# Performance work log

Hardware: AMD Instinct MI355X
Metric: run time of the kernel (lower is better)

## Reference

```python
import jax, jax.numpy as jnp
import numpy as np

NEG_SLOPE = 0.01  # torch F.leaky_relu default
N_USER = 100000
N_ITEM = 100000
N_EDGE = 640000
D = 128
N_LAYERS = 3  # 1 input + num_hidden_layers(1) + 1 output layer


def setup_inputs() -> dict:
    key = jax.random.key(0)
    ks = jax.random.split(key, 10)
    scale = 1.0 / np.sqrt(D)
    return {
        "h_user": jax.random.normal(ks[0], (N_USER, D), dtype=jnp.float32),
        "h_item": jax.random.normal(ks[1], (N_ITEM, D), dtype=jnp.float32),
        # W[layer, etype] : etype 0 = user-follows->user, 1 = user-clicks->item, 2 = item-clicked_by->user
        "W": jax.random.normal(ks[2], (N_LAYERS, 3, D, D), dtype=jnp.float32) * scale,
        "b": jnp.zeros((N_LAYERS, 3, D), dtype=jnp.float32),
        "follows_src": jax.random.randint(ks[3], (N_EDGE,), 0, N_USER, dtype=jnp.int32),
        "follows_dst": jax.random.randint(ks[4], (N_EDGE,), 0, N_USER, dtype=jnp.int32),
        "clicks_src": jax.random.randint(ks[5], (N_EDGE,), 0, N_USER, dtype=jnp.int32),
        "clicks_dst": jax.random.randint(ks[6], (N_EDGE,), 0, N_ITEM, dtype=jnp.int32),
        "cb_src": jax.random.randint(ks[7], (N_EDGE,), 0, N_ITEM, dtype=jnp.int32),
        "cb_dst": jax.random.randint(ks[8], (N_EDGE,), 0, N_USER, dtype=jnp.int32),
    }


def _etype_conv(h_src, W, b, src, dst, n_dst):
    """Per-etype Linear on src nodes, copy_u gather, mean-aggregate at dst."""
    Wh = h_src @ W + b                     # [N_src, D] dense transform (once per node)
    msg = Wh[src]                          # [E, D] gather
    s = jax.ops.segment_sum(msg, dst, num_segments=n_dst)
    cnt = jax.ops.segment_sum(jnp.ones((src.shape[0],), dtype=Wh.dtype), dst, num_segments=n_dst)
    return s / jnp.maximum(cnt, 1.0)[:, None]  # mean; isolated nodes -> 0


def _rgcn_forward(h_user, h_item, W, b, follows_src, follows_dst,
                  clicks_src, clicks_dst, cb_src, cb_dst):
    hu, hi = h_user, h_item
    for l in range(N_LAYERS):
        # per-etype mean aggregation, then cross-etype 'sum' (DGL multi_update_all)
        agg_u = (_etype_conv(hu, W[l, 0], b[l, 0], follows_src, follows_dst, N_USER)
                 + _etype_conv(hi, W[l, 2], b[l, 2], cb_src, cb_dst, N_USER))
        agg_i = _etype_conv(hu, W[l, 1], b[l, 1], clicks_src, clicks_dst, N_ITEM)
        hu = jax.nn.leaky_relu(agg_u, NEG_SLOPE)
        hi = jax.nn.leaky_relu(agg_i, NEG_SLOPE)
    return jnp.stack([hu, hi])  # [2, 100000, 128]


def reference(h_user, h_item, W, b, follows_src, follows_dst,
              clicks_src, clicks_dst, cb_src, cb_dst):
    return _rgcn_forward(h_user, h_item, W, b, follows_src, follows_dst,
                         clicks_src, clicks_dst, cb_src, cb_dst)
```

## Files before the change

kernel.cpp:

```cpp
#include <hip/hip_runtime.h>

typedef unsigned char u8;
typedef unsigned short u16;
typedef _Float16 f16;
typedef __attribute__((ext_vector_type(4))) _Float16 f16x4;
typedef __attribute__((ext_vector_type(8))) _Float16 f16x8;
typedef __attribute__((ext_vector_type(4))) float f32x4;

#define D 128
#define PG 4

__global__ __launch_bounds__(256) void k_pre(
    const float* __restrict__ h_user, const float* __restrict__ h_item,
    const float* __restrict__ W,
    const int* __restrict__ fd, const int* __restrict__ cd,
    const int* __restrict__ cbd,
    u16* __restrict__ h_all, u16* __restrict__ Wtg,
    int* __restrict__ cnt, u8* __restrict__ pos,
    int NU, int NI, int nf, int nc, int ncb,
    int nbCnt, int nbCvtU, int nbCvtI) {
  int b = blockIdx.x;
  int T = gridDim.x;
  long before = (long)b * nbCnt / T;
  long after = (long)(b + 1) * nbCnt / T;
  if (after > before) {
    int e = (int)before * 256 + threadIdx.x;
    int d;
    if (e < nf)
      d = fd[e];
    else if (e < nf + nc)
      d = NU + cd[e - nf];
    else if (e < nf + nc + ncb)
      d = NU + NI + cbd[e - nf - nc];
    else
      return;
    int p = atomicAdd(&cnt[d], 1);
    pos[e] = (u8)p;
  } else {
    int v = b - (int)before;
    if (v < nbCvtU + nbCvtI) {
      bool isU = v < nbCvtU;
      int i = (isU ? v : v - nbCvtU) * 256 + threadIdx.x;
      int n8 = (isU ? NU : NI) * 16;
      if (i >= n8) return;
      const float4* ip = (const float4*)(isU ? h_user : h_item);
      u16* op = h_all + (isU ? 0 : (size_t)NU * D);
      float4 a = ip[i * 2], c = ip[i * 2 + 1];
      f16x8 vv = {(f16)a.x, (f16)a.y, (f16)a.z, (f16)a.w,
                  (f16)c.x, (f16)c.y, (f16)c.z, (f16)c.w};
      *(f16x8*)(op + (size_t)i * 8) = vv;
    } else {
      int idx = (v - nbCvtU - nbCvtI) * 256 + threadIdx.x;
      if (idx >= 9 * 16384) return;
      int mat = idx >> 14;
      int k = (idx >> 7) & 127;
      int n = idx & 127;
      ((f16*)Wtg)[(size_t)mat * 16384 + n * 128 + k] = (f16)W[idx];
    }
  }
}

__device__ __forceinline__ int pad4(int x) { return (x + (PG - 1)) & ~(PG - 1); }

__global__ __launch_bounds__(256) void k_scanA(const int* __restrict__ cnt,
                                               int* __restrict__ part, int n) {
  int t = threadIdx.x;
  int idx = blockIdx.x * 1024 + t * 4;
  int s = 0;
  if (idx + 3 < n) {
    int4 c = *(const int4*)(cnt + idx);
    s = pad4(c.x) + pad4(c.y) + pad4(c.z) + pad4(c.w);
  } else {
#pragma unroll
    for (int j = 0; j < 4; ++j)
      if (idx + j < n) s += pad4(cnt[idx + j]);
  }
  for (int off = 1; off < 64; off <<= 1) s += __shfl_down(s, off, 64);
  __shared__ int ws[4];
  if ((t & 63) == 0) ws[t >> 6] = s;
  __syncthreads();
  if (t == 0) part[blockIdx.x] = ws[0] + ws[1] + ws[2] + ws[3];
}

__global__ __launch_bounds__(1024) void k_scanB(int* __restrict__ part, int n_part) {
  __shared__ int sh[1024];
  int t = threadIdx.x;
  int v = (t < n_part) ? part[t] : 0;
  sh[t] = v;
  __syncthreads();
  for (int off = 1; off < 1024; off <<= 1) {
    int u = (t >= off) ? sh[t - off] : 0;
    __syncthreads();
    sh[t] += u;
    __syncthreads();
  }
  if (t < n_part) part[t] = sh[t] - v;
}

__global__ __launch_bounds__(256) void k_scanC(const int* __restrict__ cnt,
                                               const int* __restrict__ part,
                                               int* __restrict__ rs, int n) {
  int t = threadIdx.x;
  int idx = blockIdx.x * 1024 + t * 4;
  int v0 = 0, v1 = 0, v2 = 0, v3 = 0;
  if (idx + 3 < n) {
    int4 c = *(const int4*)(cnt + idx);
    v0 = pad4(c.x);
    v1 = pad4(c.y);
    v2 = pad4(c.z);
    v3 = pad4(c.w);
  } else {
    if (idx < n) v0 = pad4(cnt[idx]);
    if (idx + 1 < n) v1 = pad4(cnt[idx + 1]);
    if (idx + 2 < n) v2 = pad4(cnt[idx + 2]);
    if (idx + 3 < n) v3 = pad4(cnt[idx + 3]);
  }
  int s = v0 + v1 + v2 + v3;
  int inc = s;
  int lane = t & 63, w = t >> 6;
  for (int off = 1; off < 64; off <<= 1) {
    int u = __shfl_up(inc, off, 64);
    if (lane >= off) inc += u;
  }
  __shared__ int ws[4];
  if (lane == 63) ws[w] = inc;
  __syncthreads();
  int woff = 0;
  for (int i = 0; i < w; ++i) woff += ws[i];
  int ex = part[blockIdx.x] + woff + inc - s;
  int4 r;
  r.x = ex;
  r.y = ex + v0;
  r.z = r.y + v1;
  r.w = r.z + v2;
  if (idx + 3 < n)
    *(int4*)(rs + idx) = r;
  else {
    if (idx < n) rs[idx] = r.x;
    if (idx + 1 < n) rs[idx + 1] = r.y;
    if (idx + 2 < n) rs[idx + 2] = r.z;
    if (idx + 3 < n) rs[idx + 3] = r.w;
  }
  if (idx <= n - 1 && n - 1 < idx + 4) {
    int j = n - 1 - idx;
    int incl = (j == 0) ? r.x + v0 : (j == 1) ? r.y + v1 : (j == 2) ? r.z + v2 : r.w + v3;
    rs[n] = incl;
  }
}

__global__ __launch_bounds__(256) void k_fill2(
    const int* __restrict__ fs, const int* __restrict__ fd,
    const int* __restrict__ cs, const int* __restrict__ cd,
    const int* __restrict__ cbs, const int* __restrict__ cbd,
    const int* __restrict__ rs, const int* __restrict__ cnt,
    const u8* __restrict__ pos, int* __restrict__ csr,
    int NU, int NI, int nf, int nc, int ncb, int nbFill, int N3, int ZR) {
  if ((int)blockIdx.x < nbFill) {
    int e = blockIdx.x * 256 + threadIdx.x;
    int d, s;
    if (e < nf) {
      d = fd[e];
      s = fs[e];
    } else if (e < nf + nc) {
      d = NU + cd[e - nf];
      s = cs[e - nf];
    } else if (e < nf + nc + ncb) {
      d = NU + NI + cbd[e - nf - nc];
      s = cbs[e - nf - nc] + NU;
    } else
      return;
    csr[rs[d] + (int)pos[e]] = s;
  } else {
    int d = (blockIdx.x - nbFill) * 256 + threadIdx.x;
    if (d >= N3) return;
    int deg = cnt[d];
    int degp = pad4(deg);
    int base = rs[d] + deg;
#pragma unroll
    for (int j = 0; j < PG - 1; ++j)
      if (j < degp - deg) csr[base + j] = ZR;
  }
}

__global__ __launch_bounds__(256) void k_agg3(
    const u16* __restrict__ h_all, const int* __restrict__ csr,
    const int* __restrict__ rs, const int* __restrict__ cnt,
    u16* __restrict__ M_all, int N3) {
  int wave = (blockIdx.x * 256 + threadIdx.x) >> 6;
  int lane = threadIdx.x & 63;
  int l16 = lane & 15;
  int w = wave * 4 + (lane >> 4);
  bool valid = w < N3;
  int wc = valid ? w : 0;
  int e = rs[wc];
  int en = valid ? rs[wc + 1] : e;
  int deg = valid ? cnt[wc] : 0;
  f16x8 acc0 = {0, 0, 0, 0, 0, 0, 0, 0};
  f16x8 acc1 = {0, 0, 0, 0, 0, 0, 0, 0};
  const char* hb = (const char*)h_all;
  const int4* csr4 = (const int4*)csr;
  unsigned loff = (unsigned)l16 * 16u;

  int en8 = e + ((en - e) & ~7);
  while (e < en8) {
    int4 c0 = csr4[e >> 2];
    int4 c1 = csr4[(e >> 2) + 1];
    f16x8 v0 = *(const f16x8*)(hb + ((unsigned)c0.x * 256u + loff));
    f16x8 v1 = *(const f16x8*)(hb + ((unsigned)c0.y * 256u + loff));
    f16x8 v2 = *(const f16x8*)(hb + ((unsigned)c0.z * 256u + loff));
    f16x8 v3 = *(const f16x8*)(hb + ((unsigned)c0.w * 256u + loff));
    f16x8 v4 = *(const f16x8*)(hb + ((unsigned)c1.x * 256u + loff));
    f16x8 v5 = *(const f16x8*)(hb + ((unsigned)c1.y * 256u + loff));
    f16x8 v6 = *(const f16x8*)(hb + ((unsigned)c1.z * 256u + loff));
    f16x8 v7 = *(const f16x8*)(hb + ((unsigned)c1.w * 256u + loff));
    acc0 += v0;
    acc1 += v1;
    acc0 += v2;
    acc1 += v3;
    acc0 += v4;
    acc1 += v5;
    acc0 += v6;
    acc1 += v7;
    e += 8;
  }
  if (e < en) {
    int4 c0 = csr4[e >> 2];
    f16x8 v0 = *(const f16x8*)(hb + ((unsigned)c0.x * 256u + loff));
    f16x8 v1 = *(const f16x8*)(hb + ((unsigned)c0.y * 256u + loff));
    f16x8 v2 = *(const f16x8*)(hb + ((unsigned)c0.z * 256u + loff));
    f16x8 v3 = *(const f16x8*)(hb + ((unsigned)c0.w * 256u + loff));
    acc0 += v0;
    acc1 += v1;
    acc0 += v2;
    acc1 += v3;
  }

  if (valid) {
    float invf = deg > 0 ? 1.0f / (float)deg : 0.f;
    f16 hinv = (f16)invf;
    f16x8 t = acc0 + acc1;
    f16x8 r = t * hinv;
    *(f16x8*)((char*)M_all + ((unsigned)wc * 256u + loff)) = r;
  }
}

template <int NE, int OUTF32>
__device__ __forceinline__ void gemm_body(
    const u16* __restrict__ mA, const u16* __restrict__ mBp,
    const u16* __restrict__ wtA, const u16* __restrict__ wtB,
    const float* __restrict__ bA, const float* __restrict__ bB,
    const int* __restrict__ cntA, const int* __restrict__ cntB,
    u16* __restrict__ o16, float* __restrict__ o32, int M, int blk) {
  int tid = threadIdx.x, lane = tid & 63, w = tid >> 6;
  int lr = lane & 15;
  int lk = (lane >> 4) * 8;
  long row0 = (long)blk * 128 + w * 32;

  f32x4 acc[2][8];
#pragma unroll
  for (int rt = 0; rt < 2; rt++)
#pragma unroll
    for (int n = 0; n < 8; n++) acc[rt][n] = (f32x4){0.f, 0.f, 0.f, 0.f};

#pragma unroll
  for (int e = 0; e < NE; ++e) {
    const f16* mm = (const f16*)((e == 0) ? mA : mBp);
    const f16* Wg = (const f16*)((e == 0) ? wtA : wtB);
#pragma unroll
    for (int ks = 0; ks < 4; ++ks) {
      int k0 = ks * 32 + lk;
      f16x8 bf[8];
#pragma unroll
      for (int n = 0; n < 8; n++) bf[n] = *(const f16x8*)(Wg + (n * 16 + lr) * D + k0);
#pragma unroll
      for (int rt = 0; rt < 2; rt++) {
        long r = row0 + rt * 16 + lr;
        if (r >= M) r = M - 1;
        f16x8 af = *(const f16x8*)(mm + r * D + k0);
#pragma unroll
        for (int n = 0; n < 8; n++)
          acc[rt][n] = __builtin_amdgcn_mfma_f32_16x16x32_f16(bf[n], af, acc[rt][n], 0, 0, 0);
      }
    }
  }

  int g4 = (lane >> 4) * 4;
  float4 bAr[8], bBr[8];
#pragma unroll
  for (int n = 0; n < 8; n++) {
    bAr[n] = *(const float4*)&bA[n * 16 + g4];
    if (NE == 2) bBr[n] = *(const float4*)&bB[n * 16 + g4];
  }

#pragma unroll
  for (int rt = 0; rt < 2; rt++) {
    long r = row0 + rt * 16 + lr;
    if (r < M) {
      bool mAok = cntA[r] > 0;
      bool mBok = (NE == 2) && (cntB[r] > 0);
#pragma unroll
      for (int n = 0; n < 8; n++) {
        float4 vv;
        vv.x = acc[rt][n][0];
        vv.y = acc[rt][n][1];
        vv.z = acc[rt][n][2];
        vv.w = acc[rt][n][3];
        if (mAok) {
          vv.x += bAr[n].x;
          vv.y += bAr[n].y;
          vv.z += bAr[n].z;
          vv.w += bAr[n].w;
        }
        if (mBok) {
          vv.x += bBr[n].x;
          vv.y += bBr[n].y;
          vv.z += bBr[n].z;
          vv.w += bBr[n].w;
        }
        vv.x = vv.x > 0.f ? vv.x : 0.01f * vv.x;
        vv.y = vv.y > 0.f ? vv.y : 0.01f * vv.y;
        vv.z = vv.z > 0.f ? vv.z : 0.01f * vv.z;
        vv.w = vv.w > 0.f ? vv.w : 0.01f * vv.w;
        int col = n * 16 + g4;
        if (OUTF32) {
          *(float4*)&o32[r * D + col] = vv;
        } else {
          f16x4 h = {(f16)vv.x, (f16)vv.y, (f16)vv.z, (f16)vv.w};
          *(f16x4*)((f16*)o16 + r * D + col) = h;
        }
      }
    }
  }
}

template <int OUTF32>
__global__ __launch_bounds__(256) void k_gemm2(
    const u16* __restrict__ M_all, const u16* __restrict__ Wl,
    const float* __restrict__ bl, const int* __restrict__ cnt,
    u16* __restrict__ h_all, float* __restrict__ out,
    int NU, int NI, int nbI) {
  if ((int)blockIdx.x < nbI) {
    gemm_body<1, OUTF32>(M_all + (size_t)NU * D, nullptr,
                         Wl + 16384, nullptr,
                         bl + D, nullptr,
                         cnt + NU, nullptr,
                         h_all + (size_t)NU * D, out + (size_t)NU * D, NI,
                         blockIdx.x);
  } else {
    gemm_body<2, OUTF32>(M_all, M_all + (size_t)(NU + NI) * D,
                         Wl, Wl + 2 * 16384,
                         bl, bl + 2 * D,
                         cnt, cnt + NU + NI,
                         h_all, out, NU, blockIdx.x - nbI);
  }
}

extern "C" void kernel_launch(void* const* d_in, const int* in_sizes, int n_in,
                              void* d_out, int out_size, void* d_ws, size_t ws_size,
                              hipStream_t stream) {
  const float* h_user = (const float*)d_in[0];
  const float* h_item = (const float*)d_in[1];
  const float* W = (const float*)d_in[2];
  const float* bb = (const float*)d_in[3];
  const int* f_src = (const int*)d_in[4];
  const int* f_dst = (const int*)d_in[5];
  const int* c_src = (const int*)d_in[6];
  const int* c_dst = (const int*)d_in[7];
  const int* cb_src = (const int*)d_in[8];
  const int* cb_dst = (const int*)d_in[9];

  const int NU = in_sizes[0] / D;
  const int NI = in_sizes[1] / D;
  const int nEf = in_sizes[4], nEc = in_sizes[6], nEcb = in_sizes[8];
  const int N3 = NU + NI + NU;
  const int nE = nEf + nEc + nEcb;
  const int ZR = NU + NI;

  char* p = (char*)d_ws;
  auto alloc = [&](size_t bytes) {
    char* r = p;
    p += (bytes + 255) & ~(size_t)255;
    return r;
  };
  int* cnt = (int*)alloc((size_t)N3 * 4);
  int* rs_all = (int*)alloc((size_t)(N3 + 1) * 4);
  int* part = (int*)alloc(1024 * 4);
  u16* Wtg = (u16*)alloc((size_t)9 * 16384 * 2);
  int* csr_all = (int*)alloc(((size_t)nE + (size_t)(PG - 1) * N3) * 4);
  u16* h_all = (u16*)alloc((size_t)(NU + NI + 1) * D * 2);
  u16* M_all = (u16*)alloc((size_t)N3 * D * 2);
  u8* pos = (u8*)M_all;
  (void)ws_size;

  hipMemsetAsync(cnt, 0, (size_t)N3 * 4, stream);
  hipMemsetAsync(h_all + (size_t)ZR * D, 0, D * 2, stream);

  int nbCnt = (nE + 255) / 256;
  int nbCvtU = (NU * 16 + 255) / 256;
  int nbCvtI = (NI * 16 + 255) / 256;
  int nbW = (9 * 16384 + 255) / 256;
  k_pre<<<nbCnt + nbCvtU + nbCvtI + nbW, 256, 0, stream>>>(
      h_user, h_item, W, f_dst, c_dst, cb_dst, h_all, Wtg, cnt, pos,
      NU, NI, nEf, nEc, nEcb, nbCnt, nbCvtU, nbCvtI);

  int n_part = (N3 + 1023) / 1024;
  k_scanA<<<n_part, 256, 0, stream>>>(cnt, part, N3);
  k_scanB<<<1, 1024, 0, stream>>>(part, n_part);
  k_scanC<<<n_part, 256, 0, stream>>>(cnt, part, rs_all, N3);

  int nbFill = (nE + 255) / 256;
  int nbPad = (N3 + 255) / 256;
  k_fill2<<<nbFill + nbPad, 256, 0, stream>>>(f_src, f_dst, c_src, c_dst,
                                              cb_src, cb_dst, rs_all, cnt, pos,
                                              csr_all, NU, NI, nEf, nEc, nEcb,
                                              nbFill, N3, ZR);

  int nbI = (NI + 127) / 128;
  int nbU = (NU + 127) / 128;
  int agg_blocks = ((N3 + 3) / 4 + 3) / 4;

  for (int l = 0; l < 3; ++l) {
    const u16* Wl = Wtg + (size_t)l * 3 * 16384;
    const float* bl = bb + (size_t)l * 3 * D;

    k_agg3<<<agg_blocks, 256, 0, stream>>>(h_all, csr_all, rs_all, cnt, M_all, N3);

    if (l < 2)
      k_gemm2<0><<<nbI + nbU, 256, 0, stream>>>(M_all, Wl, bl, cnt, h_all,
                                                (float*)d_out, NU, NI, nbI);
    else
      k_gemm2<1><<<nbI + nbU, 256, 0, stream>>>(M_all, Wl, bl, cnt, h_all,
                                                (float*)d_out, NU, NI, nbI);
  }
}
```

Baseline: 541.5 us.

## Pad degree counters to separate cache lines and shrink GEMM tiles to 64 rows

After: 669.8 us. +23.7%, slower.

```diff
diff --git a/kernel.cpp b/kernel.cpp
--- a/kernel.cpp
+++ b/kernel.cpp
@@ -17,7 +17,7 @@
     const int* __restrict__ cbd,
     u16* __restrict__ h_all, u16* __restrict__ Wtg,
     int* __restrict__ cnt, u8* __restrict__ pos,
-    int NU, int NI, int nf, int nc, int ncb,
+    int NU, int NI, int nf, int nc, int ncb, int S,
     int nbCnt, int nbCvtU, int nbCvtI) {
   int b = blockIdx.x;
   int T = gridDim.x;
@@ -34,7 +34,7 @@
       d = NU + NI + cbd[e - nf - nc];
     else
       return;
-    int p = atomicAdd(&cnt[d], 1);
+    int p = atomicAdd(&cnt[(size_t)d * S], 1);
     pos[e] = (u8)p;
   } else {
     int v = b - (int)before;
@@ -63,18 +63,13 @@
 __device__ __forceinline__ int pad4(int x) { return (x + (PG - 1)) & ~(PG - 1); }
 
 __global__ __launch_bounds__(256) void k_scanA(const int* __restrict__ cnt,
-                                               int* __restrict__ part, int n) {
+                                               int* __restrict__ part, int n, int S) {
   int t = threadIdx.x;
   int idx = blockIdx.x * 1024 + t * 4;
   int s = 0;
-  if (idx + 3 < n) {
-    int4 c = *(const int4*)(cnt + idx);
-    s = pad4(c.x) + pad4(c.y) + pad4(c.z) + pad4(c.w);
-  } else {
-#pragma unroll
-    for (int j = 0; j < 4; ++j)
-      if (idx + j < n) s += pad4(cnt[idx + j]);
-  }
+#pragma unroll
+  for (int j = 0; j < 4; ++j)
+    if (idx + j < n) s += pad4(cnt[(size_t)(idx + j) * S]);
   for (int off = 1; off < 64; off <<= 1) s += __shfl_down(s, off, 64);
   __shared__ int ws[4];
   if ((t & 63) == 0) ws[t >> 6] = s;
@@ -99,22 +94,14 @@
 
 __global__ __launch_bounds__(256) void k_scanC(const int* __restrict__ cnt,
                                                const int* __restrict__ part,
-                                               int* __restrict__ rs, int n) {
+                                               int* __restrict__ rs, int n, int S) {
   int t = threadIdx.x;
   int idx = blockIdx.x * 1024 + t * 4;
   int v0 = 0, v1 = 0, v2 = 0, v3 = 0;
-  if (idx + 3 < n) {
-    int4 c = *(const int4*)(cnt + idx);
-    v0 = pad4(c.x);
-    v1 = pad4(c.y);
-    v2 = pad4(c.z);
-    v3 = pad4(c.w);
-  } else {
-    if (idx < n) v0 = pad4(cnt[idx]);
-    if (idx + 1 < n) v1 = pad4(cnt[idx + 1]);
-    if (idx + 2 < n) v2 = pad4(cnt[idx + 2]);
-    if (idx + 3 < n) v3 = pad4(cnt[idx + 3]);
-  }
+  if (idx < n) v0 = pad4(cnt[(size_t)idx * S]);
+  if (idx + 1 < n) v1 = pad4(cnt[(size_t)(idx + 1) * S]);
+  if (idx + 2 < n) v2 = pad4(cnt[(size_t)(idx + 2) * S]);
+  if (idx + 3 < n) v3 = pad4(cnt[(size_t)(idx + 3) * S]);
   int s = v0 + v1 + v2 + v3;
   int inc = s;
   int lane = t & 63, w = t >> 6;
@@ -154,7 +141,7 @@
     const int* __restrict__ cbs, const int* __restrict__ cbd,
     const int* __restrict__ rs, const int* __restrict__ cnt,
     const u8* __restrict__ pos, int* __restrict__ csr,
-    int NU, int NI, int nf, int nc, int ncb, int nbFill, int N3, int ZR) {
+    int NU, int NI, int nf, int nc, int ncb, int nbFill, int N3, int ZR, int S) {
   if ((int)blockIdx.x < nbFill) {
     int e = blockIdx.x * 256 + threadIdx.x;
     int d, s;
@@ -173,7 +160,7 @@
   } else {
     int d = (blockIdx.x - nbFill) * 256 + threadIdx.x;
     if (d >= N3) return;
-    int deg = cnt[d];
+    int deg = cnt[(size_t)d * S];
     int degp = pad4(deg);
     int base = rs[d] + deg;
 #pragma unroll
@@ -185,7 +172,7 @@
 __global__ __launch_bounds__(256) void k_agg3(
     const u16* __restrict__ h_all, const int* __restrict__ csr,
     const int* __restrict__ rs, const int* __restrict__ cnt,
-    u16* __restrict__ M_all, int N3) {
+    u16* __restrict__ M_all, int N3, int S) {
   int wave = (blockIdx.x * 256 + threadIdx.x) >> 6;
   int lane = threadIdx.x & 63;
   int l16 = lane & 15;
@@ -194,7 +181,7 @@
   int wc = valid ? w : 0;
   int e = rs[wc];
   int en = valid ? rs[wc + 1] : e;
-  int deg = valid ? cnt[wc] : 0;
+  int deg = valid ? cnt[(size_t)wc * S] : 0;
   f16x8 acc0 = {0, 0, 0, 0, 0, 0, 0, 0};
   f16x8 acc1 = {0, 0, 0, 0, 0, 0, 0, 0};
   const char* hb = (const char*)h_all;
@@ -245,89 +232,51 @@
 }
 
 template <int NE, int OUTF32>
-__device__ __forceinline__ void gemm_body(
-    const u16* __restrict__ mA, const u16* __restrict__ mBp,
-    const u16* __restrict__ wtA, const u16* __restrict__ wtB,
+__device__ __forceinline__ void gemm16(
+    const u16* __restrict__ mA, const u16* __restrict__ mB2,
+    const u16* __restrict__ wA, const u16* __restrict__ wB,
     const float* __restrict__ bA, const float* __restrict__ bB,
-    const int* __restrict__ cntA, const int* __restrict__ cntB,
-    u16* __restrict__ o16, float* __restrict__ o32, int M, int blk) {
-  int tid = threadIdx.x, lane = tid & 63, w = tid >> 6;
-  int lr = lane & 15;
-  int lk = (lane >> 4) * 8;
-  long row0 = (long)blk * 128 + w * 32;
-
-  f32x4 acc[2][8];
-#pragma unroll
-  for (int rt = 0; rt < 2; rt++)
-#pragma unroll
-    for (int n = 0; n < 8; n++) acc[rt][n] = (f32x4){0.f, 0.f, 0.f, 0.f};
+    const int* __restrict__ cA, const int* __restrict__ cB, int S,
+    u16* __restrict__ ho, float* __restrict__ fo, int M, int blk) {
+  int tid = threadIdx.x, lane = tid & 63;
+  int lr = lane & 15, lk = (lane >> 4) * 8, g4 = (lane >> 4) * 4;
+  int row = blk * 64 + (tid >> 6) * 16 + lr;
+  int rowc = row < M ? row : M - 1;
+  f32x4 acc[8];
+#pragma unroll
+  for (int n = 0; n < 8; ++n) acc[n] = (f32x4){0.f, 0.f, 0.f, 0.f};
 
 #pragma unroll
   for (int e = 0; e < NE; ++e) {
-    const f16* mm = (const f16*)((e == 0) ? mA : mBp);
-    const f16* Wg = (const f16*)((e == 0) ? wtA : wtB);
+    const f16* mm = (const f16*)((e == 0) ? mA : mB2);
+    const f16* Wg = (const f16*)((e == 0) ? wA : wB);
 #pragma unroll
     for (int ks = 0; ks < 4; ++ks) {
-      int k0 = ks * 32 + lk;
-      f16x8 bf[8];
-#pragma unroll
-      for (int n = 0; n < 8; n++) bf[n] = *(const f16x8*)(Wg + (n * 16 + lr) * D + k0);
-#pragma unroll
-      for (int rt = 0; rt < 2; rt++) {
-        long r = row0 + rt * 16 + lr;
-        if (r >= M) r = M - 1;
-        f16x8 af = *(const f16x8*)(mm + r * D + k0);
-#pragma unroll
-        for (int n = 0; n < 8; n++)
-          acc[rt][n] = __builtin_amdgcn_mfma_f32_16x16x32_f16(bf[n], af, acc[rt][n], 0, 0, 0);
+      f16x8 af = *(const f16x8*)(mm + (size_t)rowc * D + ks * 32 + lk);
+#pragma unroll
+      for (int n = 0; n < 8; ++n) {
+        f16x8 bf = *(const f16x8*)(Wg + (n * 16 + lr) * D + ks * 32 + lk);
+        acc[n] = __builtin_amdgcn_mfma_f32_16x16x32_f16(bf, af, acc[n], 0, 0, 0);
       }
     }
   }
 
-  int g4 = (lane >> 4) * 4;
-  float4 bAr[8], bBr[8];
-#pragma unroll
-  for (int n = 0; n < 8; n++) {
-    bAr[n] = *(const float4*)&bA[n * 16 + g4];
-    if (NE == 2) bBr[n] = *(const float4*)&bB[n * 16 + g4];
-  }
-
-#pragma unroll
-  for (int rt = 0; rt < 2; rt++) {
-    long r = row0 + rt * 16 + lr;
-    if (r < M) {
-      bool mAok = cntA[r] > 0;
-      bool mBok = (NE == 2) && (cntB[r] > 0);
-#pragma unroll
-      for (int n = 0; n < 8; n++) {
-        float4 vv;
-        vv.x = acc[rt][n][0];
-        vv.y = acc[rt][n][1];
-        vv.z = acc[rt][n][2];
-        vv.w = acc[rt][n][3];
-        if (mAok) {
-          vv.x += bAr[n].x;
-          vv.y += bAr[n].y;
-          vv.z += bAr[n].z;
-          vv.w += bAr[n].w;
-        }
-        if (mBok) {
-          vv.x += bBr[n].x;
-          vv.y += bBr[n].y;
-          vv.z += bBr[n].z;
-          vv.w += bBr[n].w;
-        }
-        vv.x = vv.x > 0.f ? vv.x : 0.01f * vv.x;
-        vv.y = vv.y > 0.f ? vv.y : 0.01f * vv.y;
-        vv.z = vv.z > 0.f ? vv.z : 0.01f * vv.z;
-        vv.w = vv.w > 0.f ? vv.w : 0.01f * vv.w;
-        int col = n * 16 + g4;
-        if (OUTF32) {
-          *(float4*)&o32[r * D + col] = vv;
-        } else {
-          f16x4 h = {(f16)vv.x, (f16)vv.y, (f16)vv.z, (f16)vv.w};
-          *(f16x4*)((f16*)o16 + r * D + col) = h;
-        }
+  if (row < M) {
+    bool mAok = cA[(size_t)row * S] > 0;
+    bool mBok = (NE == 2) && (cB[(size_t)row * S] > 0);
+#pragma unroll
+    for (int n = 0; n < 8; ++n) {
+      int col = n * 16 + g4;
+      f32x4 vv = acc[n];
+      if (mAok) vv += *(const f32x4*)&bA[col];
+      if (mBok) vv += *(const f32x4*)&bB[col];
+#pragma unroll
+      for (int j = 0; j < 4; ++j) vv[j] = vv[j] > 0.f ? vv[j] : 0.01f * vv[j];
+      if (OUTF32) {
+        *(f32x4*)&fo[(size_t)row * D + col] = vv;
+      } else {
+        f16x4 h = {(f16)vv[0], (f16)vv[1], (f16)vv[2], (f16)vv[3]};
+        *(f16x4*)((f16*)ho + (size_t)row * D + col) = h;
       }
     }
   }
@@ -338,20 +287,20 @@
     const u16* __restrict__ M_all, const u16* __restrict__ Wl,
     const float* __restrict__ bl, const int* __restrict__ cnt,
     u16* __restrict__ h_all, float* __restrict__ out,
-    int NU, int NI, int nbI) {
+    int NU, int NI, int nbI, int S) {
   if ((int)blockIdx.x < nbI) {
-    gemm_body<1, OUTF32>(M_all + (size_t)NU * D, nullptr,
-                         Wl + 16384, nullptr,
-                         bl + D, nullptr,
-                         cnt + NU, nullptr,
-                         h_all + (size_t)NU * D, out + (size_t)NU * D, NI,
-                         blockIdx.x);
+    gemm16<1, OUTF32>(M_all + (size_t)NU * D, nullptr,
+                      Wl + 16384, nullptr,
+                      bl + D, nullptr,
+                      cnt + (size_t)NU * S, nullptr, S,
+                      h_all + (size_t)NU * D, out + (size_t)NU * D, NI,
+                      blockIdx.x);
   } else {
-    gemm_body<2, OUTF32>(M_all, M_all + (size_t)(NU + NI) * D,
-                         Wl, Wl + 2 * 16384,
-                         bl, bl + 2 * D,
-                         cnt, cnt + NU + NI,
-                         h_all, out, NU, blockIdx.x - nbI);
+    gemm16<2, OUTF32>(M_all, M_all + (size_t)(NU + NI) * D,
+                      Wl, Wl + 2 * 16384,
+                      bl, bl + 2 * D,
+                      cnt, cnt + (size_t)(NU + NI) * S, S,
+                      h_all, out, NU, blockIdx.x - nbI);
   }
 }
 
@@ -376,23 +325,30 @@
   const int nE = nEf + nEc + nEcb;
   const int ZR = NU + NI;
 
+  auto rnd = [](size_t b) { return (b + 255) & ~(size_t)255; };
+  size_t needBase = rnd((size_t)(N3 + 1) * 4) + rnd(4096) +
+                    rnd((size_t)9 * 16384 * 2) +
+                    rnd(((size_t)nE + (size_t)(PG - 1) * N3) * 4) +
+                    rnd((size_t)(NU + NI + 1) * D * 2) +
+                    rnd((size_t)N3 * D * 2);
+  int S = (needBase + rnd((size_t)N3 * 4 * 16) <= ws_size) ? 16 : 1;
+
   char* p = (char*)d_ws;
   auto alloc = [&](size_t bytes) {
     char* r = p;
     p += (bytes + 255) & ~(size_t)255;
     return r;
   };
-  int* cnt = (int*)alloc((size_t)N3 * 4);
+  int* cnt = (int*)alloc((size_t)N3 * 4 * S);
   int* rs_all = (int*)alloc((size_t)(N3 + 1) * 4);
-  int* part = (int*)alloc(1024 * 4);
+  int* part = (int*)alloc(4096);
   u16* Wtg = (u16*)alloc((size_t)9 * 16384 * 2);
   int* csr_all = (int*)alloc(((size_t)nE + (size_t)(PG - 1) * N3) * 4);
   u16* h_all = (u16*)alloc((size_t)(NU + NI + 1) * D * 2);
   u16* M_all = (u16*)alloc((size_t)N3 * D * 2);
   u8* pos = (u8*)M_all;
-  (void)ws_size;
-
-  hipMemsetAsync(cnt, 0, (size_t)N3 * 4, stream);
+
+  hipMemsetAsync(cnt, 0, (size_t)N3 * 4 * S, stream);
   hipMemsetAsync(h_all + (size_t)ZR * D, 0, D * 2, stream);
 
   int nbCnt = (nE + 255) / 256;
@@ -401,35 +357,36 @@
   int nbW = (9 * 16384 + 255) / 256;
   k_pre<<<nbCnt + nbCvtU + nbCvtI + nbW, 256, 0, stream>>>(
       h_user, h_item, W, f_dst, c_dst, cb_dst, h_all, Wtg, cnt, pos,
-      NU, NI, nEf, nEc, nEcb, nbCnt, nbCvtU, nbCvtI);
+      NU, NI, nEf, nEc, nEcb, S, nbCnt, nbCvtU, nbCvtI);
 
   int n_part = (N3 + 1023) / 1024;
-  k_scanA<<<n_part, 256, 0, stream>>>(cnt, part, N3);
+  k_scanA<<<n_part, 256, 0, stream>>>(cnt, part, N3, S);
   k_scanB<<<1, 1024, 0, stream>>>(part, n_part);
-  k_scanC<<<n_part, 256, 0, stream>>>(cnt, part, rs_all, N3);
+  k_scanC<<<n_part, 256, 0, stream>>>(cnt, part, rs_all, N3, S);
 
   int nbFill = (nE + 255) / 256;
   int nbPad = (N3 + 255) / 256;
   k_fill2<<<nbFill + nbPad, 256, 0, stream>>>(f_src, f_dst, c_src, c_dst,
                                               cb_src, cb_dst, rs_all, cnt, pos,
                                               csr_all, NU, NI, nEf, nEc, nEcb,
-                                              nbFill, N3, ZR);
-
-  int nbI = (NI + 127) / 128;
-  int nbU = (NU + 127) / 128;
+                                              nbFill, N3, ZR, S);
+
+  int nbI = (NI + 63) / 64;
+  int nbU = (NU + 63) / 64;
   int agg_blocks = ((N3 + 3) / 4 + 3) / 4;
 
   for (int l = 0; l < 3; ++l) {
     const u16* Wl = Wtg + (size_t)l * 3 * 16384;
     const float* bl = bb + (size_t)l * 3 * D;
 
-    k_agg3<<<agg_blocks, 256, 0, stream>>>(h_all, csr_all, rs_all, cnt, M_all, N3);
+    k_agg3<<<agg_blocks, 256, 0, stream>>>(h_all, csr_all, rs_all, cnt, M_all,
+                                           N3, S);
 
     if (l < 2)
       k_gemm2<0><<<nbI + nbU, 256, 0, stream>>>(M_all, Wl, bl, cnt, h_all,
-                                                (float*)d_out, NU, NI, nbI);
+                                                (float*)d_out, NU, NI, nbI, S);
     else
       k_gemm2<1><<<nbI + nbU, 256, 0, stream>>>(M_all, Wl, bl, cnt, h_all,
-                                                (float*)d_out, NU, NI, nbI);
-  }
-}
+                                                (float*)d_out, NU, NI, nbI, S);
+  }
+}
```
